# Kernel tuning notes

Hardware: AMD Instinct MI355X
Metric: run time of the kernel (lower is better)

The kernel has to match this reference:

```python
import jax, jax.numpy as jnp
import numpy as np

WS = 2          # spatial window (patch) size
C = 96          # patch channels
IMG = 256       # image size
NS = IMG // WS  # 128 patches per side
N = NS * NS     # 16384 tokens
TD = C * WS * WS  # 384 token dim
H = 6           # heads
D = TD // H     # 64 head dim
W1 = 128        # one-sided attention window (attention_window=256 // 2)
G = 50          # num global tokens
NEG = -1e9
GPOS = np.linspace(0, N - 1, G).astype(np.int32)  # torch.linspace(...).long()


def setup_inputs() -> dict:
    key = jax.random.key(0)
    ks = jax.random.split(key, 13)
    s = 1.0 / np.sqrt(TD)
    def W(k):
        return jax.random.normal(k, (TD, TD), jnp.float32) * s
    def b(k):
        return jax.random.normal(k, (TD,), jnp.float32) * 0.02
    return {
        'x': jax.random.normal(ks[0], (2, C, IMG, IMG), jnp.float32),
        'Wq': W(ks[1]), 'bq': b(ks[2]),
        'Wk': W(ks[3]), 'bk': b(ks[4]),
        'Wv': W(ks[5]), 'bv': b(ks[6]),
        'Wqg': W(ks[7]), 'bqg': b(ks[8]),
        'Wkg': W(ks[9]), 'bkg': b(ks[10]),
        'Wvg': W(ks[11]), 'bvg': b(ks[12]),
    }


def _tokens(x):
    # (B,C,IMG,IMG) -> (B,N,TD); matches unfold/permute/view of the torch code
    B = x.shape[0]
    t = x.reshape(B, C, NS, WS, NS, WS).transpose(0, 1, 2, 4, 3, 5)  # B,C,ns,ns,ws,ws
    t = t.reshape(B, C, N, WS * WS).transpose(0, 2, 1, 3)
    return t.reshape(B, N, TD)


def _untokens(o):
    B = o.shape[0]
    o = o.reshape(B, NS, NS, C, WS, WS).transpose(0, 3, 1, 4, 2, 5)
    return o.reshape(B, C, IMG, IMG)


def _heads(t):
    B = t.shape[0]
    return t.reshape(B, -1, H, D).transpose(0, 2, 1, 3)  # (B,H,S,D)


def _longformer(tokens, Wq, bq, Wk, bk, Wv, bv, Wqg, bqg, Wkg, bkg, Wvg, bvg):
    B = tokens.shape[0]
    scale = np.float32(1.0 / np.sqrt(D))
    q = _heads(tokens @ Wq + bq) * scale  # (B,H,N,D)
    k = _heads(tokens @ Wk + bk)
    v = _heads(tokens @ Wv + bv)

    nc = N // W1  # 128 chunks of size w
    qc = q.reshape(B, H, nc, W1, D)
    # overlapping key/value chunks of size 3w (prev | cur | next)
    kp = jnp.pad(k, ((0, 0), (0, 0), (W1, W1), (0, 0))).reshape(B, H, nc + 2, W1, D)
    vp = jnp.pad(v, ((0, 0), (0, 0), (W1, W1), (0, 0))).reshape(B, H, nc + 2, W1, D)
    k3 = jnp.concatenate([kp[:, :, :-2], kp[:, :, 1:-1], kp[:, :, 2:]], axis=3)  # (B,H,nc,3w,D)
    v3 = jnp.concatenate([vp[:, :, :-2], vp[:, :, 1:-1], vp[:, :, 2:]], axis=3)

    band = jnp.einsum('bhcqd,bhckd->bhcqk', qc, k3)  # (B,H,nc,w,3w)
    # banded validity: key within +-w of query, and inside [0,N)
    i = np.arange(W1)[:, None]
    j = np.arange(3 * W1)[None, :]
    rel = j - W1 - i
    relmask = (rel >= -W1) & (rel <= W1)  # (w,3w)
    absidx = np.arange(nc)[:, None] * W1 + np.arange(3 * W1)[None, :] - W1
    absmask = (absidx >= 0) & (absidx < N)  # (nc,3w)
    mask = jnp.asarray(relmask[None, :, :] & absmask[:, None, :])  # (nc,w,3w)
    band = jnp.where(mask[None, None], band, NEG)

    # global key columns seen by every (local) query
    kg = k[:, :, GPOS]  # (B,H,G,D)
    vg = v[:, :, GPOS]
    gsc = jnp.einsum('bhcqd,bhgd->bhcqg', qc, kg)  # (B,H,nc,w,G)

    probs = jax.nn.softmax(jnp.concatenate([gsc, band], axis=-1), axis=-1)
    out = jnp.einsum('bhcqg,bhgd->bhcqd', probs[..., :G], vg) \
        + jnp.einsum('bhcqk,bhckd->bhcqd', probs[..., G:], v3)
    out = out.reshape(B, H, N, D).transpose(0, 2, 1, 3).reshape(B, N, TD)

    # global-query full attention (separate projections), overwrite global rows
    qg = _heads((tokens[:, GPOS] @ Wqg + bqg)) * scale  # (B,H,G,D)
    kga = _heads(tokens @ Wkg + bkg)  # (B,H,N,D)
    vga = _heads(tokens @ Wvg + bvg)
    gp = jax.nn.softmax(jnp.einsum('bhgd,bhnd->bhgn', qg, kga), axis=-1)
    og = jnp.einsum('bhgn,bhnd->bhgd', gp, vga).transpose(0, 2, 1, 3).reshape(B, G, TD)
    return out.at[:, GPOS].set(og)


def reference(x, Wq, bq, Wk, bk, Wv, bv, Wqg, bqg, Wkg, bkg, Wvg, bvg):
    tokens = _tokens(x)
    out = _longformer(tokens, Wq, bq, Wk, bk, Wv, bv, Wqg, bqg, Wkg, bkg, Wvg, bvg)
    return _untokens(out)
```

## Files before the change

kernel.cpp:

```cpp
#include <hip/hip_runtime.h>

#define DEVI __device__ __forceinline__

typedef __bf16 v8bf __attribute__((ext_vector_type(8)));
typedef float f32x4 __attribute__((ext_vector_type(4)));
typedef int int4v __attribute__((ext_vector_type(4)));
typedef int int2v __attribute__((ext_vector_type(2)));

constexpr int B_  = 2;
constexpr int C_  = 96;
constexpr int IMG = 256;
constexpr int N_  = 16384;
constexpr int TD  = 384;
constexpr int H_  = 6;
constexpr int G_  = 50;

DEVI short f2bf(float f){
  unsigned u = __builtin_bit_cast(unsigned, f);
  u = (u + 0x7fffu + ((u >> 16) & 1u)) >> 16;
  return (short)u;
}
DEVI unsigned cvtpk(float lo, float hi){
  unsigned r;
  asm("v_cvt_pk_bf16_f32 %0, %1, %2" : "=v"(r) : "v"(lo), "v"(hi));
  return r;
}
DEVI int gpos(int g){ return (16383 * g) / 49; }

DEVI f32x4 mfma16(v8bf a, v8bf b, f32x4 c){
  return __builtin_amdgcn_mfma_f32_16x16x32_bf16(a, b, c, 0, 0, 0);
}

DEVI void gload16(const void* g, void* l){
  __builtin_amdgcn_global_load_lds((const __attribute__((address_space(1))) void*)g,
                                   (__attribute__((address_space(3))) void*)l, 16, 0, 0);
}

__global__ __launch_bounds__(256) void prep_w(
    const float* __restrict__ w0, const float* __restrict__ w1,
    const float* __restrict__ w2, const float* __restrict__ w3,
    const float* __restrict__ w4, const float* __restrict__ w5,
    short* __restrict__ Wt){
  __shared__ float sT[64][65];
  int z = blockIdx.y;
  const float* W = z==0 ? w0 : z==1 ? w1 : z==2 ? w2 : z==3 ? w3 : z==4 ? w4 : w5;
  int tile = blockIdx.x;
  int k0 = (tile / 6) * 64, n0 = (tile % 6) * 64;
  int t = threadIdx.x;
  int r = t >> 2, c0 = (t & 3) * 16;
  #pragma unroll
  for (int e = 0; e < 16; e += 4){
    f32x4 v = *reinterpret_cast<const f32x4*>(&W[(size_t)(k0+r)*TD + n0 + c0 + e]);
    #pragma unroll
    for (int i = 0; i < 4; i++) sT[r][c0 + e + i] = v[i];
  }
  __syncthreads();
  int rn = t >> 2, ck0 = (t & 3) * 16;
  short pk[16];
  #pragma unroll
  for (int e = 0; e < 16; e++) pk[e] = f2bf(sT[ck0 + e][rn]);
  short* dst = Wt + (size_t)z*TD*TD + (size_t)(n0+rn)*TD + k0 + ck0;
  *reinterpret_cast<int4v*>(dst)     = *reinterpret_cast<int4v*>(&pk[0]);
  *reinterpret_cast<int4v*>(dst + 8) = *reinterpret_cast<int4v*>(&pk[8]);
}

__global__ __launch_bounds__(256) void tokenize(const float* __restrict__ x,
                                                short* __restrict__ tokens){
  __shared__ float sX[24][2][260];
  int p = blockIdx.x, cq = blockIdx.y, b = blockIdx.z;
  int tid = threadIdx.x;
  #pragma unroll
  for (int it = 0; it < 12; it++){
    int u = it*256 + tid;
    int c_l = u >> 7, rem = u & 127, r = rem >> 6, j4 = rem & 63;
    f32x4 v = *reinterpret_cast<const f32x4*>(
        &x[(((size_t)b*C_ + cq*24 + c_l)*IMG + 2*p + r)*IMG + j4*4]);
    *reinterpret_cast<f32x4*>(&sX[c_l][r][j4*4]) = v;
  }
  __syncthreads();
  #pragma unroll
  for (int it = 0; it < 6; it++){
    int v = it*256 + tid;
    int nsj = v / 12, ck = v % 12;
    short o[8];
    #pragma unroll
    for (int e = 0; e < 8; e++){
      int tl = ck*8 + e;
      int c_l = tl >> 2, wi = (tl >> 1) & 1, wj = tl & 1;
      o[e] = f2bf(sX[c_l][wi][2*nsj + wj]);
    }
    *reinterpret_cast<int4v*>(tokens + ((size_t)b*N_ + p*128 + nsj)*TD + cq*96 + ck*8)
        = *reinterpret_cast<int4v*>(o);
  }
}

__global__ __launch_bounds__(256) void gemm_proj(
    const short* __restrict__ A, const short* __restrict__ Wt,
    const float* __restrict__ bq, const float* __restrict__ bk, const float* __restrict__ bv,
    const float* __restrict__ bkg, const float* __restrict__ bvg, const float* __restrict__ bqg,
    short* __restrict__ qbuf, short* __restrict__ kbuf, short* __restrict__ vT,
    short* __restrict__ kgabuf, short* __restrict__ vgaT, short* __restrict__ qgb)
{
  __shared__ short smem[16384];
  int lin = blockIdx.x;
  int mt, by, bz;
  if (lin < 3840){
    int id = (lin & 7)*480 + (lin >> 3);
    mt = id / 15; int r15 = id % 15;
    by = r15 % 3; bz = r15 / 3;
  } else {
    int id2 = lin - 3840;
    if (id2 >= 3) return;
    mt = 0; by = id2; bz = 5;
  }
  const float* bias = bz==0 ? bq : bz==1 ? bk : bz==2 ? bv : bz==3 ? bkg : bz==4 ? bvg : bqg;
  const short* Wz = Wt + bz*TD*TD;
  int m0 = mt * 128, n0 = by * 128;
  int tid = threadIdx.x, l = tid & 63, w = tid >> 6;
  int wm = w >> 1, wn = w & 1;
  int q16 = l & 15, g4 = l >> 4;
  bool trans = (bz == 2 || bz == 4);
  bool is_qg = (bz == 5);

  int st_r  = (l >> 2);
  int st_cg = ((l & 3) ^ ((l >> 3) & 3));
  auto STAGE = [&](int kt, int s){
    #pragma unroll
    for (int it = 0; it < 4; it++){
      int ch = w*4 + it;
      int c8 = ch & 7;
      int r_ = c8*16 + st_r;
      const short* src;
      if (ch < 8){
        const short* abase;
        if (is_qg){
          int bq_ = r_ >> 6, qq = r_ & 63;
          abase = A + ((size_t)bq_*N_ + gpos(qq < G_ ? qq : 0))*TD;
        } else {
          abase = A + (size_t)(m0+r_)*TD;
        }
        src = abase + kt*32 + st_cg*8;
      } else {
        src = Wz + (size_t)(n0+r_)*TD + kt*32 + st_cg*8;
      }
      gload16(src, smem + ((ch < 8) ? 0 : 8192) + s*4096 + c8*512);
    }
  };

  int fr = q16;
  int fcg = g4 ^ ((l >> 1) & 3);
  f32x4 acc[4][4] = {};

  STAGE(0, 0);
  if (trans){
    #pragma unroll 2
    for (int t = 0; t < 12; t++){
      int cur = t & 1;
      if (t < 11){ STAGE(t+1, cur ^ 1); asm volatile("s_waitcnt vmcnt(4)" ::: "memory"); }
      else       { asm volatile("s_waitcnt vmcnt(0)" ::: "memory"); }
      __builtin_amdgcn_s_barrier();
      v8bf af[4], bfr[4];
      #pragma unroll
      for (int i = 0; i < 4; i++){
        af[i]  = *reinterpret_cast<const v8bf*>(&smem[       cur*4096 + (wm*64 + i*16 + fr)*32 + fcg*8]);
        bfr[i] = *reinterpret_cast<const v8bf*>(&smem[8192 + cur*4096 + (wn*64 + i*16 + fr)*32 + fcg*8]);
      }
      #pragma unroll
      for (int mi = 0; mi < 4; mi++)
        #pragma unroll
        for (int ni = 0; ni < 4; ni++)
          acc[mi][ni] = mfma16(af[mi], bfr[ni], acc[mi][ni]);
      asm volatile("s_waitcnt lgkmcnt(0)" ::: "memory");
      __builtin_amdgcn_s_barrier();
    }
    short* outT = (bz == 2) ? vT : vgaT;
    #pragma unroll
    for (int mi = 0; mi < 4; mi++){
      int n_base = wm*64 + mi*16 + g4*4;
      #pragma unroll
      for (int ni = 0; ni < 4; ni++){
        int t_local = wn*64 + ni*16 + q16;
        float bc = bias[n0 + t_local];
        short pk[4];
        #pragma unroll
        for (int jj = 0; jj < 4; jj++) pk[jj] = f2bf(acc[mi][ni][jj] + bc);
        int phys = t_local*128 + (((n_base >> 3) ^ (t_local & 15)) << 3) + (n_base & 7);
        *reinterpret_cast<int2v*>(&smem[phys]) = *reinterpret_cast<int2v*>(pk);
      }
    }
    __syncthreads();
    int b = mt >> 7;
    int nb = m0 & 16383;
    #pragma unroll
    for (int p = 0; p < 8; p++){
      int t = p*16 + (tid >> 4);
      int c8 = tid & 15;
      int4v val = *reinterpret_cast<const int4v*>(&smem[t*128 + ((c8 ^ (t & 15)) << 3)]);
      int h = (n0 + t) >> 6, d = (n0 + t) & 63;
      *reinterpret_cast<int4v*>(outT + ((size_t)((b*H_ + h)*64 + d))*N_ + nb + c8*8) = val;
    }
  } else {
    #pragma unroll 2
    for (int t = 0; t < 12; t++){
      int cur = t & 1;
      if (t < 11){ STAGE(t+1, cur ^ 1); asm volatile("s_waitcnt vmcnt(4)" ::: "memory"); }
      else       { asm volatile("s_waitcnt vmcnt(0)" ::: "memory"); }
      __builtin_amdgcn_s_barrier();
      v8bf af[4], bfr[4];
      #pragma unroll
      for (int i = 0; i < 4; i++){
        af[i]  = *reinterpret_cast<const v8bf*>(&smem[       cur*4096 + (wm*64 + i*16 + fr)*32 + fcg*8]);
        bfr[i] = *reinterpret_cast<const v8bf*>(&smem[8192 + cur*4096 + (wn*64 + i*16 + fr)*32 + fcg*8]);
      }
      #pragma unroll
      for (int mi = 0; mi < 4; mi++)
        #pragma unroll
        for (int ni = 0; ni < 4; ni++)
          acc[mi][ni] = mfma16(bfr[ni], af[mi], acc[mi][ni]);
      asm volatile("s_waitcnt lgkmcnt(0)" ::: "memory");
      __builtin_amdgcn_s_barrier();
    }
    short* out = bz==0 ? qbuf : bz==1 ? kbuf : bz==3 ? kgabuf : qgb;
    float scale = (bz == 0 || bz == 5) ? 0.125f : 1.0f;
    #pragma unroll
    for (int mi = 0; mi < 4; mi++){
      int tl = wm*64 + mi*16 + q16;
      int x = (tl & 7) << 1;
      #pragma unroll
      for (int ni = 0; ni < 4; ni++){
        int tdl = wn*64 + ni*16 + g4*4;
        f32x4 bvv = *reinterpret_cast<const f32x4*>(&bias[n0 + tdl]);
        short pk[4];
        #pragma unroll
        for (int jj = 0; jj < 4; jj++) pk[jj] = f2bf((acc[mi][ni][jj] + bvv[jj]) * scale);
        int c4 = (tdl >> 2) ^ x;
        *reinterpret_cast<int2v*>(&smem[tl*128 + c4*4]) = *reinterpret_cast<int2v*>(pk);
      }
    }
    __syncthreads();
    #pragma unroll
    for (int p = 0; p < 8; p++){
      int r = p*16 + (tid >> 4);
      int c16 = tid & 15;
      int c4 = (2*c16) ^ ((r & 7) << 1);
      int4v val = *reinterpret_cast<const int4v*>(&smem[r*128 + c4*4]);
      *reinterpret_cast<int4v*>(out + (size_t)(m0 + r)*TD + n0 + c16*8) = val;
    }
  }
}

__global__ void gather_gkv(const short* __restrict__ kbuf, const short* __restrict__ vT,
                           short* __restrict__ kg, short* __restrict__ vgTg){
  int bh = blockIdx.x; int b = bh / H_, h = bh % H_;
  int t = threadIdx.x;
  #pragma unroll
  for (int it = 0; it < 2; it++){
    int u = it*256 + t; int g = u >> 3, cc = (u & 7)*8;
    int4v val = {};
    if (g < G_) val = *reinterpret_cast<const int4v*>(kbuf + ((size_t)b*N_ + gpos(g))*TD + h*64 + cc);
    *reinterpret_cast<int4v*>(kg + (size_t)bh*4096 + g*64 + cc) = val;
  }
  #pragma unroll
  for (int it = 0; it < 16; it++){
    int u = it*256 + t; int d = u >> 6, g = u & 63;
    short val = 0;
    if (g < G_) val = vT[((size_t)bh*64 + d)*N_ + gpos(g)];
    vgTg[(size_t)bh*4096 + d*64 + g] = val;
  }
}

__global__ __launch_bounds__(512, 4) void band_attn(
    const short* __restrict__ qb, const short* __restrict__ kbuf, const short* __restrict__ vT,
    const short* __restrict__ kg, const short* __restrict__ vgTg,
    float* __restrict__ out)
{
  __shared__ short sK[448][64];
  __shared__ short sP[8][16][72];
  int lin = blockIdx.y*128 + blockIdx.x;
  int id = (lin & 7)*192 + (lin >> 3);
  int c = id & 127;
  int bh = id >> 7; int b = bh / H_, h = bh % H_;
  int tid = threadIdx.x, l = tid & 63, w = tid >> 6;
  int g4 = l >> 4, q16 = l & 15;
  int cb0 = c*128 - 128;

  #pragma unroll
  for (int it = 0; it < 7; it++){
    int ch = w*7 + it;
    int r = ch*8 + (l>>3);
    int cc = ((l & 7) ^ (l >> 3)) * 8;
    const short* src;
    if (ch < 8){
      src = kg + (size_t)bh*4096 + r*64 + cc;
    } else {
      int ka = cb0 + r - 64;
      ka = ka < 0 ? 0 : (ka > N_-1 ? N_-1 : ka);
      src = kbuf + ((size_t)b*N_ + ka)*TD + h*64 + cc;
    }
    gload16(src, &sK[ch*8][0]);
  }

  int qrow0 = c*128 + w*16;
  v8bf aq[2];
  #pragma unroll
  for (int s = 0; s < 2; s++)
    aq[s] = *reinterpret_cast<const v8bf*>(qb + ((size_t)b*N_ + qrow0 + q16)*TD + h*64 + s*32 + g4*8);

  __syncthreads();

  f32x4 o[4] = {};
  float mrun = -1e30f, lrun = 0.f;
  int sbase = w >> 2;
  int i_ = w*16 + q16;

  auto QK = [&](int rbase, f32x4* sc){
    v8bf bkf[4][2];
    #pragma unroll
    for (int kc = 0; kc < 4; kc++)
      #pragma unroll
      for (int s = 0; s < 2; s++)
        bkf[kc][s] = *reinterpret_cast<const v8bf*>(
            &sK[rbase + kc*16 + q16][(((s << 2) | g4) ^ (q16 & 7)) * 8]);
    __builtin_amdgcn_s_setprio(1);
    #pragma unroll
    for (int kc = 0; kc < 4; kc++){
      sc[kc] = mfma16(bkf[kc][0], aq[0], sc[kc]);
      sc[kc] = mfma16(bkf[kc][1], aq[1], sc[kc]);
    }
    __builtin_amdgcn_s_setprio(0);
  };

  for (int ph = 0; ph < 3; ph++){
    int s0bA = (sbase + 2*ph - 1) * 64;
    int s0bB = (sbase + 2*ph) * 64;
    bool isgA = (ph == 0);
    int kabsA = cb0 + s0bA, kabsB = cb0 + s0bB;
    bool validA = isgA || (kabsA >= 0 && kabsA < N_);
    bool validB = (kabsB >= 0 && kabsB < N_);
    if (!validA && !validB) continue;

    f32x4 sc[8];
    const f32x4 negv = {-1e30f, -1e30f, -1e30f, -1e30f};
    #pragma unroll
    for (int j = 0; j < 8; j++) sc[j] = negv;

    if (validA){
      sc[0] = sc[1] = sc[2] = sc[3] = f32x4{0.f, 0.f, 0.f, 0.f};
      QK(isgA ? 0 : 64 + s0bA, &sc[0]);
      if (isgA){
        #pragma unroll
        for (int jj = 0; jj < 4; jj++)
          if (48 + g4*4 + jj >= G_) sc[3][jj] = -1e30f;
      } else {
        bool allv = (s0bA >= w*16 + 15) && (s0bA <= w*16 + 193);
        if (!allv){
          #pragma unroll
          for (int kc = 0; kc < 4; kc++)
            #pragma unroll
            for (int jj = 0; jj < 4; jj++){
              int rel = s0bA + kc*16 + g4*4 + jj - 128 - i_;
              if (rel < -128 || rel > 128) sc[kc][jj] = -1e30f;
            }
        }
      }
    }
    if (validB){
      sc[4] = sc[5] = sc[6] = sc[7] = f32x4{0.f, 0.f, 0.f, 0.f};
      QK(64 + s0bB, &sc[4]);
      bool allv = (s0bB >= w*16 + 15) && (s0bB <= w*16 + 193);
      if (!allv){
        #pragma unroll
        for (int kc = 0; kc < 4; kc++)
          #pragma unroll
          for (int jj = 0; jj < 4; jj++){
            int rel = s0bB + kc*16 + g4*4 + jj - 128 - i_;
            if (rel < -128 || rel > 128) sc[4+kc][jj] = -1e30f;
          }
      }
    }
    float mk = -1e30f;
    #pragma unroll
    for (int j = 0; j < 8; j++)
      #pragma unroll
      for (int jj = 0; jj < 4; jj++) mk = fmaxf(mk, sc[j][jj]);
    mk = fmaxf(mk, __shfl_xor(mk, 16, 64));
    mk = fmaxf(mk, __shfl_xor(mk, 32, 64));
    if (__any(mk > mrun + 8.f)){
      float mnew = fmaxf(mrun, mk);
      float f_ = __expf(mrun - mnew);
      mrun = mnew;
      lrun *= f_;
      #pragma unroll
      for (int cf = 0; cf < 4; cf++)
        #pragma unroll
        for (int jj = 0; jj < 4; jj++) o[cf][jj] *= f_;
    }
    float s_ = 0.f;
    #pragma unroll
    for (int j = 0; j < 8; j++)
      #pragma unroll
      for (int jj = 0; jj < 4; jj++){
        sc[j][jj] = __expf(sc[j][jj] - mrun);
        s_ += sc[j][jj];
      }
    s_ += __shfl_xor(s_, 16, 64);
    s_ += __shfl_xor(s_, 32, 64);
    lrun += s_;
    if (validA){
      #pragma unroll
      for (int kc = 0; kc < 4; kc++){
        int2v pw = { (int)cvtpk(sc[kc][0], sc[kc][1]), (int)cvtpk(sc[kc][2], sc[kc][3]) };
        *reinterpret_cast<int2v*>(&sP[w][q16][kc*16 + g4*4]) = pw;
      }
      v8bf ap[2];
      #pragma unroll
      for (int s2 = 0; s2 < 2; s2++)
        ap[s2] = *reinterpret_cast<const v8bf*>(&sP[w][q16][s2*32 + g4*8]);
      #pragma unroll
      for (int s2 = 0; s2 < 2; s2++){
        v8bf bv[4];
        #pragma unroll
        for (int cf = 0; cf < 4; cf++){
          const short* vsrc = isgA
            ? vgTg + (size_t)bh*4096 + (cf*16 + q16)*64 + s2*32 + g4*8
            : vT + ((size_t)bh*64 + cf*16 + q16)*N_ + kabsA + s2*32 + g4*8;
          bv[cf] = *reinterpret_cast<const v8bf*>(vsrc);
        }
        __builtin_amdgcn_s_setprio(1);
        #pragma unroll
        for (int cf = 0; cf < 4; cf++) o[cf] = mfma16(bv[cf], ap[s2], o[cf]);
        __builtin_amdgcn_s_setprio(0);
      }
    }
    if (validB){
      #pragma unroll
      for (int kc = 0; kc < 4; kc++){
        int2v pw = { (int)cvtpk(sc[4+kc][0], sc[4+kc][1]), (int)cvtpk(sc[4+kc][2], sc[4+kc][3]) };
        *reinterpret_cast<int2v*>(&sP[w][q16][kc*16 + g4*4]) = pw;
      }
      v8bf ap[2];
      #pragma unroll
      for (int s2 = 0; s2 < 2; s2++)
        ap[s2] = *reinterpret_cast<const v8bf*>(&sP[w][q16][s2*32 + g4*8]);
      #pragma unroll
      for (int s2 = 0; s2 < 2; s2++){
        v8bf bv[4];
        #pragma unroll
        for (int cf = 0; cf < 4; cf++)
          bv[cf] = *reinterpret_cast<const v8bf*>(
              vT + ((size_t)bh*64 + cf*16 + q16)*N_ + kabsB + s2*32 + g4*8);
        __builtin_amdgcn_s_setprio(1);
        #pragma unroll
        for (int cf = 0; cf < 4; cf++) o[cf] = mfma16(bv[cf], ap[s2], o[cf]);
        __builtin_amdgcn_s_setprio(0);
      }
    }
  }
  float inv = 1.0f / lrun;
  int n = qrow0 + q16;
  int i0 = (n >> 7)*2, j0 = (n & 127)*2;
  #pragma unroll
  for (int cf = 0; cf < 4; cf++)
    #pragma unroll
    for (int jj = 0; jj < 4; jj++){
      float val = o[cf][jj] * inv;
      int t_ = h*64 + cf*16 + g4*4 + jj;
      int cc = t_ >> 2, wi = (t_ >> 1) & 1, wj = t_ & 1;
      out[((b*C_ + cc)*IMG + i0 + wi)*IMG + j0 + wj] = val;
    }
}

__global__ __launch_bounds__(256) void gattn_partial(
    const short* __restrict__ qgb, const short* __restrict__ kga, const short* __restrict__ vgaT,
    float* __restrict__ gpart)
{
  __shared__ short sP[4][64][72];
  int bh = blockIdx.x; int b = bh / H_, h = bh % H_;
  int kc = blockIdx.y;
  int tid = threadIdx.x, l = tid & 63, w = tid >> 6;
  int g4 = l >> 4, q16 = l & 15;
  v8bf aq[4][2];
  #pragma unroll
  for (int rf = 0; rf < 4; rf++)
    #pragma unroll
    for (int s = 0; s < 2; s++)
      aq[rf][s] = *reinterpret_cast<const v8bf*>(qgb + (b*64 + rf*16 + q16)*TD + h*64 + s*32 + g4*8);
  f32x4 o[4][4] = {};
  float mrun[4], lrun[4];
  #pragma unroll
  for (int rf = 0; rf < 4; rf++){ mrun[rf] = -1e30f; lrun[rf] = 0.f; }
  int keybase = kc*1024 + w*256;
  for (int st = 0; st < 4; st++){
    int key0 = keybase + st*64;
    v8bf bkf[4][2];
    #pragma unroll
    for (int kcf = 0; kcf < 4; kcf++)
      #pragma unroll
      for (int s = 0; s < 2; s++)
        bkf[kcf][s] = *reinterpret_cast<const v8bf*>(kga + ((size_t)b*N_ + key0 + kcf*16 + q16)*TD + h*64 + s*32 + g4*8);
    v8bf bv[4][2];
    #pragma unroll
    for (int cf = 0; cf < 4; cf++)
      #pragma unroll
      for (int s2 = 0; s2 < 2; s2++)
        bv[cf][s2] = *reinterpret_cast<const v8bf*>(vgaT + ((size_t)bh*64 + cf*16 + q16)*N_ + key0 + s2*32 + g4*8);
    #pragma unroll
    for (int rf = 0; rf < 4; rf++){
      f32x4 sc[4] = {};
      #pragma unroll
      for (int kcf = 0; kcf < 4; kcf++){
        sc[kcf] = mfma16(bkf[kcf][0], aq[rf][0], sc[kcf]);
        sc[kcf] = mfma16(bkf[kcf][1], aq[rf][1], sc[kcf]);
      }
      float mk = -1e30f;
      #pragma unroll
      for (int kcf = 0; kcf < 4; kcf++)
        #pragma unroll
        for (int jj = 0; jj < 4; jj++) mk = fmaxf(mk, sc[kcf][jj]);
      mk = fmaxf(mk, __shfl_xor(mk, 16, 64));
      mk = fmaxf(mk, __shfl_xor(mk, 32, 64));
      float mnew = fmaxf(mrun[rf], mk);
      float f_ = __expf(mrun[rf] - mnew);
      mrun[rf] = mnew;
      float s_ = 0.f;
      #pragma unroll
      for (int kcf = 0; kcf < 4; kcf++){
        #pragma unroll
        for (int jj = 0; jj < 4; jj++){
          sc[kcf][jj] = __expf(sc[kcf][jj] - mnew);
          s_ += sc[kcf][jj];
        }
        int2v pw = { (int)cvtpk(sc[kcf][0], sc[kcf][1]), (int)cvtpk(sc[kcf][2], sc[kcf][3]) };
        *reinterpret_cast<int2v*>(&sP[w][rf*16 + q16][kcf*16 + g4*4]) = pw;
      }
      s_ += __shfl_xor(s_, 16, 64);
      s_ += __shfl_xor(s_, 32, 64);
      lrun[rf] = lrun[rf]*f_ + s_;
      #pragma unroll
      for (int cf = 0; cf < 4; cf++)
        #pragma unroll
        for (int jj = 0; jj < 4; jj++) o[rf][cf][jj] *= f_;
    }
    #pragma unroll
    for (int rf = 0; rf < 4; rf++){
      v8bf ap[2];
      #pragma unroll
      for (int s2 = 0; s2 < 2; s2++)
        ap[s2] = *reinterpret_cast<const v8bf*>(&sP[w][rf*16 + q16][s2*32 + g4*8]);
      #pragma unroll
      for (int cf = 0; cf < 4; cf++){
        o[rf][cf] = mfma16(bv[cf][0], ap[0], o[rf][cf]);
        o[rf][cf] = mfma16(bv[cf][1], ap[1], o[rf][cf]);
      }
    }
  }
  float* base = gpart + (size_t)(bh*64 + kc*4 + w) * 4224;
  #pragma unroll
  for (int rf = 0; rf < 4; rf++){
    if (g4 == 0){ base[rf*16 + q16] = mrun[rf]; base[64 + rf*16 + q16] = lrun[rf]; }
    #pragma unroll
    for (int cf = 0; cf < 4; cf++)
      #pragma unroll
      for (int jj = 0; jj < 4; jj++)
        base[128 + (cf*16 + g4*4 + jj)*64 + rf*16 + q16] = o[rf][cf][jj];
  }
}

__global__ void gattn_combine(const float* __restrict__ gpart, float* __restrict__ out){
  int bh = blockIdx.x; int b = bh / H_, h = bh % H_;
  int t = threadIdx.x;
  int q = t & 63;
  int d = blockIdx.y*4 + (t >> 6);
  if (q >= G_) return;
  const float* pb = gpart + (size_t)bh * 64 * 4224;
  float M = -1e30f;
  for (int p = 0; p < 64; p++) M = fmaxf(M, pb[p*4224 + q]);
  float L = 0.f; float acc = 0.f;
  for (int p = 0; p < 64; p++){
    const float* pp = pb + p*4224;
    float wgt = __expf(pp[q] - M);
    L += pp[64 + q] * wgt;
    acc += pp[128 + d*64 + q] * wgt;
  }
  float invL = 1.0f / L;
  int n = gpos(q);
  int i0 = (n >> 7)*2, j0 = (n & 127)*2;
  int t_ = h*64 + d;
  int cc = t_ >> 2, wi = (t_ >> 1) & 1, wj = t_ & 1;
  out[((b*C_ + cc)*IMG + i0 + wi)*IMG + j0 + wj] = acc * invL;
}

extern "C" void kernel_launch(void* const* d_in, const int* in_sizes, int n_in,
                              void* d_out, int out_size, void* d_ws, size_t ws_size,
                              hipStream_t stream)
{
  (void)in_sizes; (void)n_in; (void)out_size; (void)ws_size;
  const float* x   = (const float*)d_in[0];
  const float* Wq  = (const float*)d_in[1];  const float* bq  = (const float*)d_in[2];
  const float* Wk  = (const float*)d_in[3];  const float* bk  = (const float*)d_in[4];
  const float* Wv  = (const float*)d_in[5];  const float* bv  = (const float*)d_in[6];
  const float* Wqg = (const float*)d_in[7];  const float* bqg = (const float*)d_in[8];
  const float* Wkg = (const float*)d_in[9];  const float* bkg = (const float*)d_in[10];
  const float* Wvg = (const float*)d_in[11]; const float* bvg = (const float*)d_in[12];
  float* out = (float*)d_out;

  short* ws = (short*)d_ws;
  const size_t SZ = (size_t)B_ * N_ * TD;
  short* tokens  = ws;
  short* Wt      = tokens  + SZ;
  short* qgb     = Wt      + (size_t)6*TD*TD;
  short* qbuf    = qgb     + (size_t)128*TD;
  short* kbuf    = qbuf    + SZ;
  short* kgabuf  = kbuf    + SZ;
  short* vT      = kgabuf  + SZ;
  short* vgaT    = vT      + SZ;
  short* kg      = vgaT    + SZ;
  short* vgTg    = kg      + (size_t)12*64*64;
  float* gpart   = (float*)tokens;

  prep_w<<<dim3(36,6), dim3(256), 0, stream>>>(Wq, Wk, Wv, Wkg, Wvg, Wqg, Wt);
  tokenize<<<dim3(128,4,2), dim3(256), 0, stream>>>(x, tokens);
  gemm_proj<<<dim3(3848), dim3(256), 0, stream>>>(tokens, Wt, bq, bk, bv, bkg, bvg, bqg,
                                                  qbuf, kbuf, vT, kgabuf, vgaT, qgb);
  gather_gkv<<<dim3(12), dim3(256), 0, stream>>>(kbuf, vT, kg, vgTg);
  band_attn<<<dim3(128,12), dim3(512), 0, stream>>>(qbuf, kbuf, vT, kg, vgTg, out);
  gattn_partial<<<dim3(12,16), dim3(256), 0, stream>>>(qgb, kgabuf, vgaT, gpart);
  gattn_combine<<<dim3(12,16), dim3(256), 0, stream>>>(gpart, out);
}
```

Before: 207.1 us.

## Fuse global-query attention partials into band attention launch and widen gather

Folds the global-query partial attention into the band attention kernel as 192 extra blocks appended to a flattened 1D grid. Each 512-thread block splits the work into 8 waves covering half the query rows each, and reuses the band kernel's shared memory for the probability tile. The goal is to drop one kernel launch and let the global-attention blocks run alongside the tail of the band blocks. The global K/V gather is also spread over 16x more blocks with scalar per-element loads, so it is less serialized. In exchange, the band kernel's register and occupancy profile now has to cover the extra code path.

```diff
diff --git a/kernel.cpp b/kernel.cpp
--- a/kernel.cpp
+++ b/kernel.cpp
@@ -251,37 +251,135 @@
 
 __global__ void gather_gkv(const short* __restrict__ kbuf, const short* __restrict__ vT,
                            short* __restrict__ kg, short* __restrict__ vgTg){
-  int bh = blockIdx.x; int b = bh / H_, h = bh % H_;
+  int bh = blockIdx.x; int s = blockIdx.y;
+  int b = bh / H_, h = bh % H_;
   int t = threadIdx.x;
-  #pragma unroll
-  for (int it = 0; it < 2; it++){
-    int u = it*256 + t; int g = u >> 3, cc = (u & 7)*8;
-    int4v val = {};
-    if (g < G_) val = *reinterpret_cast<const int4v*>(kbuf + ((size_t)b*N_ + gpos(g))*TD + h*64 + cc);
-    *reinterpret_cast<int4v*>(kg + (size_t)bh*4096 + g*64 + cc) = val;
-  }
-  #pragma unroll
-  for (int it = 0; it < 16; it++){
-    int u = it*256 + t; int d = u >> 6, g = u & 63;
+  {
+    int d = s*4 + (t >> 6), g = t & 63;
     short val = 0;
     if (g < G_) val = vT[((size_t)bh*64 + d)*N_ + gpos(g)];
     vgTg[(size_t)bh*4096 + d*64 + g] = val;
   }
+  {
+    int g = s*4 + (t >> 6), c = t & 63;
+    short val = 0;
+    if (g < G_) val = kbuf[((size_t)b*N_ + gpos(g))*TD + h*64 + c];
+    kg[(size_t)bh*4096 + g*64 + c] = val;
+  }
 }
 
 __global__ __launch_bounds__(512, 4) void band_attn(
     const short* __restrict__ qb, const short* __restrict__ kbuf, const short* __restrict__ vT,
     const short* __restrict__ kg, const short* __restrict__ vgTg,
-    float* __restrict__ out)
+    const short* __restrict__ qgb, const short* __restrict__ kga, const short* __restrict__ vgaT,
+    float* __restrict__ gpart, float* __restrict__ out)
 {
   __shared__ short sK[448][64];
   __shared__ short sP[8][16][72];
-  int lin = blockIdx.y*128 + blockIdx.x;
+  int lin = blockIdx.x;
+  int tid = threadIdx.x, l = tid & 63, w = tid >> 6;
+  int g4 = l >> 4, q16 = l & 15;
+
+  if (lin >= 1536){
+    int gb = lin - 1536;
+    int bh2 = gb >> 4, kcg = gb & 15;
+    int b2 = bh2 / H_, h2 = bh2 % H_;
+    int wr = w >> 1, qh = w & 1;
+    int rec = kcg*4 + wr;
+    short* sp2 = &sK[0][0] + w*2304;
+    v8bf aq2[2][2];
+    #pragma unroll
+    for (int rf2 = 0; rf2 < 2; rf2++)
+      #pragma unroll
+      for (int s = 0; s < 2; s++)
+        aq2[rf2][s] = *reinterpret_cast<const v8bf*>(
+            qgb + (b2*64 + (qh*2+rf2)*16 + q16)*TD + h2*64 + s*32 + g4*8);
+    f32x4 o2[2][4] = {};
+    float mr[2] = {-1e30f, -1e30f}, lr[2] = {0.f, 0.f};
+    int keybase = rec*256;
+    for (int st = 0; st < 4; st++){
+      int key0 = keybase + st*64;
+      v8bf bkf[4][2];
+      #pragma unroll
+      for (int kcf = 0; kcf < 4; kcf++)
+        #pragma unroll
+        for (int s = 0; s < 2; s++)
+          bkf[kcf][s] = *reinterpret_cast<const v8bf*>(
+              kga + ((size_t)b2*N_ + key0 + kcf*16 + q16)*TD + h2*64 + s*32 + g4*8);
+      #pragma unroll
+      for (int rf2 = 0; rf2 < 2; rf2++){
+        f32x4 sc[4] = {};
+        #pragma unroll
+        for (int kcf = 0; kcf < 4; kcf++){
+          sc[kcf] = mfma16(bkf[kcf][0], aq2[rf2][0], sc[kcf]);
+          sc[kcf] = mfma16(bkf[kcf][1], aq2[rf2][1], sc[kcf]);
+        }
+        float mk = -1e30f;
+        #pragma unroll
+        for (int kcf = 0; kcf < 4; kcf++)
+          #pragma unroll
+          for (int jj = 0; jj < 4; jj++) mk = fmaxf(mk, sc[kcf][jj]);
+        mk = fmaxf(mk, __shfl_xor(mk, 16, 64));
+        mk = fmaxf(mk, __shfl_xor(mk, 32, 64));
+        float mnew = fmaxf(mr[rf2], mk);
+        float f_ = __expf(mr[rf2] - mnew);
+        mr[rf2] = mnew;
+        float s_ = 0.f;
+        #pragma unroll
+        for (int kcf = 0; kcf < 4; kcf++){
+          #pragma unroll
+          for (int jj = 0; jj < 4; jj++){
+            sc[kcf][jj] = __expf(sc[kcf][jj] - mnew);
+            s_ += sc[kcf][jj];
+          }
+          int2v pw = { (int)cvtpk(sc[kcf][0], sc[kcf][1]), (int)cvtpk(sc[kcf][2], sc[kcf][3]) };
+          *reinterpret_cast<int2v*>(&sp2[(rf2*16 + q16)*72 + kcf*16 + g4*4]) = pw;
+        }
+        s_ += __shfl_xor(s_, 16, 64);
+        s_ += __shfl_xor(s_, 32, 64);
+        lr[rf2] = lr[rf2]*f_ + s_;
+        #pragma unroll
+        for (int cf = 0; cf < 4; cf++)
+          #pragma unroll
+          for (int jj = 0; jj < 4; jj++) o2[rf2][cf][jj] *= f_;
+      }
+      v8bf bv[4][2];
+      #pragma unroll
+      for (int cf = 0; cf < 4; cf++)
+        #pragma unroll
+        for (int s2 = 0; s2 < 2; s2++)
+          bv[cf][s2] = *reinterpret_cast<const v8bf*>(
+              vgaT + ((size_t)bh2*64 + cf*16 + q16)*N_ + key0 + s2*32 + g4*8);
+      #pragma unroll
+      for (int rf2 = 0; rf2 < 2; rf2++){
+        v8bf ap[2];
+        #pragma unroll
+        for (int s2 = 0; s2 < 2; s2++)
+          ap[s2] = *reinterpret_cast<const v8bf*>(&sp2[(rf2*16 + q16)*72 + s2*32 + g4*8]);
+        #pragma unroll
+        for (int cf = 0; cf < 4; cf++){
+          o2[rf2][cf] = mfma16(bv[cf][0], ap[0], o2[rf2][cf]);
+          o2[rf2][cf] = mfma16(bv[cf][1], ap[1], o2[rf2][cf]);
+        }
+      }
+    }
+    float* base = gpart + (size_t)(bh2*64 + rec) * 4224;
+    #pragma unroll
+    for (int rf2 = 0; rf2 < 2; rf2++){
+      int rf = qh*2 + rf2;
+      if (g4 == 0){ base[rf*16 + q16] = mr[rf2]; base[64 + rf*16 + q16] = lr[rf2]; }
+      #pragma unroll
+      for (int cf = 0; cf < 4; cf++)
+        #pragma unroll
+        for (int jj = 0; jj < 4; jj++)
+          base[128 + (cf*16 + g4*4 + jj)*64 + rf*16 + q16] = o2[rf2][cf][jj];
+    }
+    return;
+  }
+
   int id = (lin & 7)*192 + (lin >> 3);
   int c = id & 127;
   int bh = id >> 7; int b = bh / H_, h = bh % H_;
-  int tid = threadIdx.x, l = tid & 63, w = tid >> 6;
-  int g4 = l >> 4, q16 = l & 15;
   int cb0 = c*128 - 128;
 
   #pragma unroll
@@ -468,102 +566,6 @@
       int cc = t_ >> 2, wi = (t_ >> 1) & 1, wj = t_ & 1;
       out[((b*C_ + cc)*IMG + i0 + wi)*IMG + j0 + wj] = val;
     }
-}
-
-__global__ __launch_bounds__(256) void gattn_partial(
-    const short* __restrict__ qgb, const short* __restrict__ kga, const short* __restrict__ vgaT,
-    float* __restrict__ gpart)
-{
-  __shared__ short sP[4][64][72];
-  int bh = blockIdx.x; int b = bh / H_, h = bh % H_;
-  int kc = blockIdx.y;
-  int tid = threadIdx.x, l = tid & 63, w = tid >> 6;
-  int g4 = l >> 4, q16 = l & 15;
-  v8bf aq[4][2];
-  #pragma unroll
-  for (int rf = 0; rf < 4; rf++)
-    #pragma unroll
-    for (int s = 0; s < 2; s++)
-      aq[rf][s] = *reinterpret_cast<const v8bf*>(qgb + (b*64 + rf*16 + q16)*TD + h*64 + s*32 + g4*8);
-  f32x4 o[4][4] = {};
-  float mrun[4], lrun[4];
-  #pragma unroll
-  for (int rf = 0; rf < 4; rf++){ mrun[rf] = -1e30f; lrun[rf] = 0.f; }
-  int keybase = kc*1024 + w*256;
-  for (int st = 0; st < 4; st++){
-    int key0 = keybase + st*64;
-    v8bf bkf[4][2];
-    #pragma unroll
-    for (int kcf = 0; kcf < 4; kcf++)
-      #pragma unroll
-      for (int s = 0; s < 2; s++)
-        bkf[kcf][s] = *reinterpret_cast<const v8bf*>(kga + ((size_t)b*N_ + key0 + kcf*16 + q16)*TD + h*64 + s*32 + g4*8);
-    v8bf bv[4][2];
-    #pragma unroll
-    for (int cf = 0; cf < 4; cf++)
-      #pragma unroll
-      for (int s2 = 0; s2 < 2; s2++)
-        bv[cf][s2] = *reinterpret_cast<const v8bf*>(vgaT + ((size_t)bh*64 + cf*16 + q16)*N_ + key0 + s2*32 + g4*8);
-    #pragma unroll
-    for (int rf = 0; rf < 4; rf++){
-      f32x4 sc[4] = {};
-      #pragma unroll
-      for (int kcf = 0; kcf < 4; kcf++){
-        sc[kcf] = mfma16(bkf[kcf][0], aq[rf][0], sc[kcf]);
-        sc[kcf] = mfma16(bkf[kcf][1], aq[rf][1], sc[kcf]);
-      }
-      float mk = -1e30f;
-      #pragma unroll
-      for (int kcf = 0; kcf < 4; kcf++)
-        #pragma unroll
-        for (int jj = 0; jj < 4; jj++) mk = fmaxf(mk, sc[kcf][jj]);
-      mk = fmaxf(mk, __shfl_xor(mk, 16, 64));
-      mk = fmaxf(mk, __shfl_xor(mk, 32, 64));
-      float mnew = fmaxf(mrun[rf], mk);
-      float f_ = __expf(mrun[rf] - mnew);
-      mrun[rf] = mnew;
-      float s_ = 0.f;
-      #pragma unroll
-      for (int kcf = 0; kcf < 4; kcf++){
-        #pragma unroll
-        for (int jj = 0; jj < 4; jj++){
-          sc[kcf][jj] = __expf(sc[kcf][jj] - mnew);
-          s_ += sc[kcf][jj];
-        }
-        int2v pw = { (int)cvtpk(sc[kcf][0], sc[kcf][1]), (int)cvtpk(sc[kcf][2], sc[kcf][3]) };
-        *reinterpret_cast<int2v*>(&sP[w][rf*16 + q16][kcf*16 + g4*4]) = pw;
-      }
-      s_ += __shfl_xor(s_, 16, 64);
-      s_ += __shfl_xor(s_, 32, 64);
-      lrun[rf] = lrun[rf]*f_ + s_;
-      #pragma unroll
-      for (int cf = 0; cf < 4; cf++)
-        #pragma unroll
-        for (int jj = 0; jj < 4; jj++) o[rf][cf][jj] *= f_;
-    }
-    #pragma unroll
-    for (int rf = 0; rf < 4; rf++){
-      v8bf ap[2];
-      #pragma unroll
-      for (int s2 = 0; s2 < 2; s2++)
-        ap[s2] = *reinterpret_cast<const v8bf*>(&sP[w][rf*16 + q16][s2*32 + g4*8]);
-      #pragma unroll
-      for (int cf = 0; cf < 4; cf++){
-        o[rf][cf] = mfma16(bv[cf][0], ap[0], o[rf][cf]);
-        o[rf][cf] = mfma16(bv[cf][1], ap[1], o[rf][cf]);
-      }
-    }
-  }
-  float* base = gpart + (size_t)(bh*64 + kc*4 + w) * 4224;
-  #pragma unroll
-  for (int rf = 0; rf < 4; rf++){
-    if (g4 == 0){ base[rf*16 + q16] = mrun[rf]; base[64 + rf*16 + q16] = lrun[rf]; }
-    #pragma unroll
-    for (int cf = 0; cf < 4; cf++)
-      #pragma unroll
-      for (int jj = 0; jj < 4; jj++)
-        base[128 + (cf*16 + g4*4 + jj)*64 + rf*16 + q16] = o[rf][cf][jj];
-  }
 }
 
 __global__ void gattn_combine(const float* __restrict__ gpart, float* __restrict__ out){
@@ -622,8 +624,8 @@
   tokenize<<<dim3(128,4,2), dim3(256), 0, stream>>>(x, tokens);
   gemm_proj<<<dim3(3848), dim3(256), 0, stream>>>(tokens, Wt, bq, bk, bv, bkg, bvg, bqg,
                                                   qbuf, kbuf, vT, kgabuf, vgaT, qgb);
-  gather_gkv<<<dim3(12), dim3(256), 0, stream>>>(kbuf, vT, kg, vgTg);
-  band_attn<<<dim3(128,12), dim3(512), 0, stream>>>(qbuf, kbuf, vT, kg, vgTg, out);
-  gattn_partial<<<dim3(12,16), dim3(256), 0, stream>>>(qgb, kgabuf, vgaT, gpart);
+  gather_gkv<<<dim3(12,16), dim3(256), 0, stream>>>(kbuf, vT, kg, vgTg);
+  band_attn<<<dim3(1728), dim3(512), 0, stream>>>(qbuf, kbuf, vT, kg, vgTg,
+                                                  qgb, kgabuf, vgaT, gpart, out);
   gattn_combine<<<dim3(12,16), dim3(256), 0, stream>>>(gpart, out);
 }
```

New measurement: 204.8 us, median of 2. No clear change (-1.1%).
